# Performance work log

Hardware: AMD Instinct MI355X
Metric: run time of the kernel (lower is better)

The kernel has to match this reference:

```python
import jax, jax.numpy as jnp
import numpy as np

D_MODEL, N_HEADS = 768, 12
D_K = D_MODEL // N_HEADS
NEG = -1e9


def setup_inputs() -> dict:
    key = jax.random.key(0)
    ks = jax.random.split(key, 12)
    B, S, D = 2, 4096, D_MODEL
    s = 1.0 / np.sqrt(D)
    inp = {
        'query': jax.random.normal(ks[0], (B, S, D), jnp.float32),
        'key': jax.random.normal(ks[1], (B, S, D), jnp.float32),
        'value': jax.random.normal(ks[2], (B, S, D), jnp.float32),
        'mask': jnp.ones((B, S), jnp.int32),
        'Wq': jax.random.normal(ks[3], (D, D), jnp.float32) * s,
        'bq': jnp.zeros((D,), jnp.float32),
        'Wk': jax.random.normal(ks[4], (D, D), jnp.float32) * s,
        'bk': jnp.zeros((D,), jnp.float32),
        'Wv': jax.random.normal(ks[5], (D, D), jnp.float32) * s,
        'bv': jnp.zeros((D,), jnp.float32),
        'Wo': jax.random.normal(ks[6], (D, D), jnp.float32) * s,
        'bo': jnp.zeros((D,), jnp.float32),
    }
    return inp


def reference(query, key, value, mask, Wq, bq, Wk, bk, Wv, bv, Wo, bo):
    B, Sq, D = query.shape
    Sk = key.shape[1]
    # torch Linear: x @ W.T + b; weights stored [out, in]
    def proj(x, W, b, S):
        return (x @ W.T + b).reshape(B, S, N_HEADS, D_K).transpose(0, 2, 1, 3)
    Q = proj(query, Wq, bq, Sq)   # [B,H,Sq,Dk]
    K = proj(key, Wk, bk, Sk)
    V = proj(value, Wv, bv, Sk)
    scores = jnp.einsum('bhqd,bhkd->bhqk', Q, K) / jnp.sqrt(jnp.float32(D_K))
    # padding mask on keys: [B,1,1,Sk]
    scores = jnp.where(mask[:, None, None, :] == 0, NEG, scores)
    # causal mask (triu, diagonal=1)
    causal = jnp.triu(jnp.ones((Sq, Sk), bool), k=1)
    scores = jnp.where(causal[None, None], NEG, scores)
    attn = jax.nn.softmax(scores, axis=-1)
    out = jnp.einsum('bhqk,bhkd->bhqd', attn, V)
    out = out.transpose(0, 2, 1, 3).reshape(B, Sq, D)
    return out @ Wo.T + bo
```

## Files before the change

### kernel.cpp

```cpp
#include <hip/hip_runtime.h>
#include <hip/hip_bf16.h>

#define D_MODEL 768
#define N_HEADS 12
#define D_K     64
#define NEG_INF (-1e9f)
#define SCALE_Q 0.1803368801111154f
#define W_ELEMS (D_MODEL * D_MODEL)

typedef __attribute__((ext_vector_type(8))) short          bf16x8;
typedef __attribute__((ext_vector_type(4))) float          floatx4;
typedef __attribute__((ext_vector_type(4))) unsigned short ushortx4;
typedef __attribute__((ext_vector_type(2))) unsigned int   uintx2;
typedef __attribute__((ext_vector_type(4))) unsigned int   uintx4;

static __device__ __forceinline__ unsigned short f2bf(float f) {
    unsigned u = __builtin_bit_cast(unsigned, f);
    u += 0x7FFFu + ((u >> 16) & 1u);
    return (unsigned short)(u >> 16);
}

static __device__ __forceinline__ float exp2_hw(float x) {
#if __has_builtin(__builtin_amdgcn_exp2f)
    return __builtin_amdgcn_exp2f(x);
#else
    return __builtin_exp2f(x);
#endif
}

static __device__ __forceinline__ float rcp_hw(float x) {
#if __has_builtin(__builtin_amdgcn_rcpf)
    return __builtin_amdgcn_rcpf(x);
#else
    return 1.f / x;
#endif
}

static __device__ __forceinline__ void gload_lds16(const void* g, void* l) {
    __builtin_amdgcn_global_load_lds(
        (const __attribute__((address_space(1))) void*)g,
        (__attribute__((address_space(3))) void*)l, 16, 0, 0);
}

__global__ __launch_bounds__(256) void convert_w4(
    const float* __restrict__ W0, const float* __restrict__ W1,
    const float* __restrict__ W2, const float* __restrict__ W3,
    unsigned short* __restrict__ out)
{
    const float* src[4] = {W0, W1, W2, W3};
    const float* W = src[blockIdx.y];
    unsigned short* o = out + (size_t)blockIdx.y * W_ELEMS;
    const int i = (blockIdx.x * 256 + threadIdx.x) * 4;
    float4 v = *(const float4*)(W + i);
    ushortx4 h = { f2bf(v.x), f2bf(v.y), f2bf(v.z), f2bf(v.w) };
    *(ushortx4*)(o + i) = h;
}

__global__ __launch_bounds__(256) void convert_a3(
    const float* __restrict__ A0, const float* __restrict__ A1,
    const float* __restrict__ A2,
    unsigned short* __restrict__ O0, unsigned short* __restrict__ O1,
    unsigned short* __restrict__ O2)
{
    const int z = blockIdx.y;
    const float* A = (z == 0) ? A0 : (z == 1) ? A1 : A2;
    unsigned short* O = (z == 0) ? O0 : (z == 1) ? O1 : O2;
    const int i = (blockIdx.x * 256 + threadIdx.x) * 4;
    float4 v = *(const float4*)(A + i);
    ushortx4 h = { f2bf(v.x), f2bf(v.y), f2bf(v.z), f2bf(v.w) };
    *(ushortx4*)(O + i) = h;
}

__global__ __launch_bounds__(256) void gemm128(
    const unsigned short* __restrict__ A0, const unsigned short* __restrict__ A1,
    const unsigned short* __restrict__ A2,
    const unsigned short* __restrict__ W0, const unsigned short* __restrict__ W1,
    const unsigned short* __restrict__ W2,
    const float* __restrict__ b0, const float* __restrict__ b1,
    const float* __restrict__ b2,
    void* __restrict__ C0, void* __restrict__ C1, void* __restrict__ C2,
    int S)
{
    __shared__ __align__(16) unsigned short As[2][128 * 32];
    __shared__ __align__(16) unsigned short Bs[2][128 * 32];

    const int z = blockIdx.z;
    const unsigned short* A = (z == 0) ? A0 : (z == 1) ? A1 : A2;
    const unsigned short* W = (z == 0) ? W0 : (z == 1) ? W1 : W2;
    const float* bias       = (z == 0) ? b0 : (z == 1) ? b1 : b2;
    void* C                 = (z == 0) ? C0 : (z == 1) ? C1 : C2;
    const float scale = (z == 0) ? SCALE_Q : 1.0f;
    const int mode = (z == 2) ? 3 : 1;

    const int tid  = threadIdx.x;
    const int wave = tid >> 6;
    const int lane = tid & 63;
    const int quad = lane >> 4;
    const int l16  = lane & 15;
    const int m0 = blockIdx.x * 128;
    const int n0 = blockIdx.y * 128;
    const int wm = (wave & 1) * 64;
    const int wn = (wave >> 1) * 64;
    const int sr = lane >> 2;
    const int sc = (lane & 3) << 3;

    const floatx4 zero4 = {0.f, 0.f, 0.f, 0.f};
    floatx4 acc[4][4];
    #pragma unroll
    for (int i = 0; i < 4; ++i)
        #pragma unroll
        for (int j = 0; j < 4; ++j) acc[i][j] = zero4;

    #pragma unroll
    for (int c = 0; c < 2; ++c) {
        const int row = wave * 32 + c * 16;
        gload_lds16(A + (size_t)(m0 + row + sr) * D_MODEL + sc,
                    As[0] + row * 32);
        gload_lds16(W + (size_t)(n0 + row + sr) * D_MODEL + sc,
                    Bs[0] + row * 32);
    }
    __syncthreads();

    const int NI = D_MODEL / 32;
    for (int it = 0; it < NI; ++it) {
        const int cur = it & 1;

        if (it + 1 < NI) {
            const int kn = (it + 1) * 32;
            #pragma unroll
            for (int c = 0; c < 2; ++c) {
                const int row = wave * 32 + c * 16;
                gload_lds16(A + (size_t)(m0 + row + sr) * D_MODEL + kn + sc,
                            As[cur ^ 1] + row * 32);
                gload_lds16(W + (size_t)(n0 + row + sr) * D_MODEL + kn + sc,
                            Bs[cur ^ 1] + row * 32);
            }
        }

        bf16x8 af[4], bfr[4];
        #pragma unroll
        for (int i = 0; i < 4; ++i)
            af[i] = *(const bf16x8*)(As[cur] + (wm + i * 16 + l16) * 32 + quad * 8);
        #pragma unroll
        for (int j = 0; j < 4; ++j)
            bfr[j] = *(const bf16x8*)(Bs[cur] + (wn + j * 16 + l16) * 32 + quad * 8);
        #pragma unroll
        for (int i = 0; i < 4; ++i)
            #pragma unroll
            for (int j = 0; j < 4; ++j)
                acc[i][j] = __builtin_amdgcn_mfma_f32_16x16x32_bf16(
                    bfr[j], af[i], acc[i][j], 0, 0, 0);
        __syncthreads();
    }

    #pragma unroll
    for (int i = 0; i < 4; ++i) {
        const int m = m0 + wm + i * 16 + l16;
        #pragma unroll
        for (int j = 0; j < 4; ++j) {
            const int nb = n0 + wn + j * 16 + quad * 4;
            const float4 bv = *(const float4*)(bias + nb);
            float v0 = (acc[i][j][0] + bv.x) * scale;
            float v1 = (acc[i][j][1] + bv.y) * scale;
            float v2 = (acc[i][j][2] + bv.z) * scale;
            float v3 = (acc[i][j][3] + bv.w) * scale;
            if (mode == 1) {
                ushortx4 o = {f2bf(v0), f2bf(v1), f2bf(v2), f2bf(v3)};
                *(ushortx4*)((unsigned short*)C + (size_t)m * D_MODEL + nb) = o;
            } else {
                const int bb = m / S, s = m - bb * S;
                const int hh = nb >> 6, d = nb & 63;
                unsigned short* base = (unsigned short*)C +
                    ((size_t)(bb * N_HEADS + hh) * D_K + d) * S + s;
                base[0]         = f2bf(v0);
                base[(size_t)S]     = f2bf(v1);
                base[(size_t)S * 2] = f2bf(v2);
                base[(size_t)S * 3] = f2bf(v3);
            }
        }
    }
}

__global__ __launch_bounds__(256) void gemm64o(
    const unsigned short* __restrict__ A,
    const unsigned short* __restrict__ W,
    const float* __restrict__ bias,
    float* __restrict__ C)
{
    __shared__ __align__(16) unsigned short As[2][64 * 32];
    __shared__ __align__(16) unsigned short Bs[2][128 * 32];

    const int tid  = threadIdx.x;
    const int wave = tid >> 6;
    const int lane = tid & 63;
    const int quad = lane >> 4;
    const int l16  = lane & 15;
    const int m0 = blockIdx.x * 64;
    const int n0 = blockIdx.y * 128;
    const int wn = wave * 32;
    const int sr = lane >> 2;
    const int sc = (lane & 3) << 3;

    const floatx4 zero4 = {0.f, 0.f, 0.f, 0.f};
    floatx4 acc[4][2];
    #pragma unroll
    for (int i = 0; i < 4; ++i)
        #pragma unroll
        for (int j = 0; j < 2; ++j) acc[i][j] = zero4;

    {
        if (wave < 2) {
            const int g0 = wave * 32;
            gload_lds16(A + (size_t)(m0 + g0 + sr) * D_MODEL + sc,
                        As[0] + g0 * 32);
            gload_lds16(A + (size_t)(m0 + g0 + 16 + sr) * D_MODEL + sc,
                        As[0] + (g0 + 16) * 32);
            const int bg = 96 + wave * 16;
            gload_lds16(W + (size_t)(n0 + bg + sr) * D_MODEL + sc,
                        Bs[0] + bg * 32);
        } else {
            const int bg = (wave - 2) * 48;
            #pragma unroll
            for (int c = 0; c < 3; ++c)
                gload_lds16(W + (size_t)(n0 + bg + c * 16 + sr) * D_MODEL + sc,
                            Bs[0] + (bg + c * 16) * 32);
        }
    }
    __syncthreads();

    const int NI = D_MODEL / 32;
    for (int it = 0; it < NI; ++it) {
        const int cur = it & 1;

        if (it + 1 < NI) {
            const int kn = (it + 1) * 32;
            if (wave < 2) {
                const int g0 = wave * 32;
                gload_lds16(A + (size_t)(m0 + g0 + sr) * D_MODEL + kn + sc,
                            As[cur ^ 1] + g0 * 32);
                gload_lds16(A + (size_t)(m0 + g0 + 16 + sr) * D_MODEL + kn + sc,
                            As[cur ^ 1] + (g0 + 16) * 32);
                const int bg = 96 + wave * 16;
                gload_lds16(W + (size_t)(n0 + bg + sr) * D_MODEL + kn + sc,
                            Bs[cur ^ 1] + bg * 32);
            } else {
                const int bg = (wave - 2) * 48;
                #pragma unroll
                for (int c = 0; c < 3; ++c)
                    gload_lds16(W + (size_t)(n0 + bg + c * 16 + sr) * D_MODEL + kn + sc,
                                Bs[cur ^ 1] + (bg + c * 16) * 32);
            }
        }

        bf16x8 af[4], bfr[2];
        #pragma unroll
        for (int i = 0; i < 4; ++i)
            af[i] = *(const bf16x8*)(As[cur] + (i * 16 + l16) * 32 + quad * 8);
        #pragma unroll
        for (int j = 0; j < 2; ++j)
            bfr[j] = *(const bf16x8*)(Bs[cur] + (wn + j * 16 + l16) * 32 + quad * 8);
        #pragma unroll
        for (int i = 0; i < 4; ++i)
            #pragma unroll
            for (int j = 0; j < 2; ++j)
                acc[i][j] = __builtin_amdgcn_mfma_f32_16x16x32_bf16(
                    bfr[j], af[i], acc[i][j], 0, 0, 0);
        __syncthreads();
    }

    #pragma unroll
    for (int i = 0; i < 4; ++i) {
        const int m = m0 + i * 16 + l16;
        #pragma unroll
        for (int j = 0; j < 2; ++j) {
            const int nb = n0 + wn + j * 16 + quad * 4;
            const float4 bv = *(const float4*)(bias + nb);
            float4 o = {acc[i][j][0] + bv.x, acc[i][j][1] + bv.y,
                        acc[i][j][2] + bv.z, acc[i][j][3] + bv.w};
            *(float4*)(C + (size_t)m * D_MODEL + nb) = o;
        }
    }
}

__global__ __launch_bounds__(256) void flash_attn(
    const unsigned short* __restrict__ Qp,
    const unsigned short* __restrict__ Kp,
    const unsigned short* __restrict__ VpT,
    const int* __restrict__ mask,
    unsigned short* __restrict__ O,
    int S)
{
    __shared__ __align__(16) unsigned short Ks [2][64 * 64];
    __shared__ __align__(16) unsigned short Vts[2][64 * 64];
    __shared__ __align__(16) float mskf[2][64];

    const int L  = blockIdx.x;
    const int bh = L % 24;
    const int p  = L / 24;
    const int h  = bh % 12;
    const int b  = bh / 12;
    const int nqt = S >> 6;
    const int tid  = threadIdx.x;
    const int wave = tid >> 6;
    const int lane = tid & 63;
    const int quad = lane >> 4;
    const int l16  = lane & 15;
    const int sx   = (l16 & 7) << 3;
    const int qh   = wave & 1;
    const int kh2  = wave >> 1;

    const unsigned short* Kbase = Kp  + (size_t)(b * S) * D_MODEL + h * D_K;
    const unsigned short* Vbase = VpT + (size_t)(b * N_HEADS + h) * D_K * S;
    const int* mbase = mask + b * S;

    const int srow = wave * 8 + (lane >> 3);
    const int sgc  = ((lane & 7) ^ (lane >> 3)) << 3;

    const floatx4 zero4 = {0.f, 0.f, 0.f, 0.f};
    const short one_bf = (short)0x3F80;
    const bf16x8 ones = {one_bf, one_bf, one_bf, one_bf,
                         one_bf, one_bf, one_bf, one_bf};

    #pragma unroll
    for (int sel = 0; sel < 2; ++sel) {
        const int qt = sel ? (nqt - 1 - p) : p;
        const int q0 = qt * 64;

        bf16x8 qf[2][2];
        #pragma unroll
        for (int qg = 0; qg < 2; ++qg) {
            const size_t rowQ =
                (size_t)(b * S + q0 + qh * 32 + qg * 16 + l16) * D_MODEL + h * D_K;
            qf[qg][0] = *(const bf16x8*)(Qp + rowQ + quad * 8);
            qf[qg][1] = *(const bf16x8*)(Qp + rowQ + 32 + quad * 8);
        }

        floatx4 acc2[2][4];
        floatx4 accl[2];
        #pragma unroll
        for (int qg = 0; qg < 2; ++qg) {
            accl[qg] = zero4;
            #pragma unroll
            for (int dt = 0; dt < 4; ++dt) acc2[qg][dt] = zero4;
        }

        const int ni = qt + 1;

        #pragma unroll
        for (int c = 0; c < 2; ++c) {
            gload_lds16(Kbase + (size_t)(c * 32 + srow) * D_MODEL + sgc,
                        (char*)Ks[0] + (c * 4 + wave) * 1024);
            gload_lds16(Vbase + (size_t)(c * 32 + srow) * S + sgc,
                        (char*)Vts[0] + (c * 4 + wave) * 1024);
        }
        if (tid < 64) mskf[0][tid] = (mbase[tid] == 0) ? NEG_INF : 0.f;
        __syncthreads();

        for (int kt = 0; kt < ni; ++kt) {
            const int k0 = kt * 64;
            const int cur = kt & 1;

            if (kt + 1 < ni) {
                const int kn = k0 + 64;
                #pragma unroll
                for (int c = 0; c < 2; ++c) {
                    gload_lds16(
                        Kbase + (size_t)(kn + c * 32 + srow) * D_MODEL + sgc,
                        (char*)Ks[cur ^ 1] + (c * 4 + wave) * 1024);
                    gload_lds16(
                        Vbase + (size_t)(c * 32 + srow) * S + kn + sgc,
                        (char*)Vts[cur ^ 1] + (c * 4 + wave) * 1024);
                }
                if (tid < 64)
                    mskf[cur ^ 1][tid] = (mbase[kn + tid] == 0) ? NEG_INF : 0.f;
            }

            floatx4 s[2][2];
            __builtin_amdgcn_s_setprio(1);
            #pragma unroll
            for (int nt = 0; nt < 2; ++nt) {
                const int krow = kh2 * 32 + nt * 16 + l16;
                const unsigned short* kro = Ks[cur] + krow * 64;
                const bf16x8 kf0 = *(const bf16x8*)(kro + ((quad * 8) ^ sx));
                const bf16x8 kf1 = *(const bf16x8*)(kro + ((32 + quad * 8) ^ sx));
                const floatx4 cm =
                    *(const floatx4*)(&mskf[cur][kh2 * 32 + nt * 16 + quad * 4]);
                #pragma unroll
                for (int qg = 0; qg < 2; ++qg) {
                    floatx4 c = cm;
                    c = __builtin_amdgcn_mfma_f32_16x16x32_bf16(kf0, qf[qg][0], c, 0, 0, 0);
                    c = __builtin_amdgcn_mfma_f32_16x16x32_bf16(kf1, qf[qg][1], c, 0, 0, 0);
                    s[nt][qg] = c;
                }
            }
            __builtin_amdgcn_s_setprio(0);

            if (kt == ni - 1) {
                #pragma unroll
                for (int nt = 0; nt < 2; ++nt) {
                    const int kb = k0 + kh2 * 32 + nt * 16 + quad * 4;
                    #pragma unroll
                    for (int qg = 0; qg < 2; ++qg) {
                        const int qa = q0 + qh * 32 + qg * 16 + l16;
                        #pragma unroll
                        for (int r = 0; r < 4; ++r)
                            if (kb + r > qa) s[nt][qg][r] = NEG_INF;
                    }
                }
            }

            unsigned pk0[2][2], pk1[2][2];
            #pragma unroll
            for (int nt = 0; nt < 2; ++nt)
                #pragma unroll
                for (int qg = 0; qg < 2; ++qg) {
                    const float e0 = exp2_hw(s[nt][qg][0]);
                    const float e1 = exp2_hw(s[nt][qg][1]);
                    const float e2 = exp2_hw(s[nt][qg][2]);
                    const float e3 = exp2_hw(s[nt][qg][3]);
                    pk0[nt][qg] = __builtin_amdgcn_perm(
                        __builtin_bit_cast(unsigned, e1),
                        __builtin_bit_cast(unsigned, e0), 0x07060302u);
                    pk1[nt][qg] = __builtin_amdgcn_perm(
                        __builtin_bit_cast(unsigned, e3),
                        __builtin_bit_cast(unsigned, e2), 0x07060302u);
                }

            bf16x8 pf[2];
            #pragma unroll
            for (int qg = 0; qg < 2; ++qg) {
                uintx2 a32 = __builtin_amdgcn_permlane32_swap(
                    pk0[0][qg], pk0[1][qg], false, false);
                uintx2 b32 = __builtin_amdgcn_permlane32_swap(
                    pk1[0][qg], pk1[1][qg], false, false);
                uintx2 a16 = __builtin_amdgcn_permlane16_swap(
                    a32[0], a32[1], false, false);
                uintx2 b16 = __builtin_amdgcn_permlane16_swap(
                    b32[0], b32[1], false, false);
                const uintx4 pw = {a16[0], b16[0], a16[1], b16[1]};
                pf[qg] = __builtin_bit_cast(bf16x8, pw);
            }
            __builtin_amdgcn_s_setprio(1);
            #pragma unroll
            for (int dt = 0; dt < 4; ++dt) {
                const int vcol = (kh2 * 32 + quad * 8) ^ sx;
                const bf16x8 vf =
                    *(const bf16x8*)(Vts[cur] + (dt * 16 + l16) * 64 + vcol);
                #pragma unroll
                for (int qg = 0; qg < 2; ++qg)
                    acc2[qg][dt] = __builtin_amdgcn_mfma_f32_16x16x32_bf16(
                        pf[qg], vf, acc2[qg][dt], 0, 0, 0);
            }
            #pragma unroll
            for (int qg = 0; qg < 2; ++qg)
                accl[qg] = __builtin_amdgcn_mfma_f32_16x16x32_bf16(
                    pf[qg], ones, accl[qg], 0, 0, 0);
            __builtin_amdgcn_s_setprio(0);

            __syncthreads();
        }

        float* Kf = (float*)Ks;
        float* Vf = (float*)Vts;
        if (kh2 == 1) {
            #pragma unroll
            for (int qg = 0; qg < 2; ++qg) {
                #pragma unroll
                for (int dt = 0; dt < 4; ++dt)
                    *(floatx4*)(Kf + (qh * 8 + qg * 4 + dt) * 256 + lane * 4) =
                        acc2[qg][dt];
                *(floatx4*)(Vf + (qh * 2 + qg) * 256 + lane * 4) = accl[qg];
            }
        }
        __syncthreads();
        if (kh2 == 0) {
            #pragma unroll
            for (int qg = 0; qg < 2; ++qg) {
                accl[qg] += *(const floatx4*)(Vf + (qh * 2 + qg) * 256 + lane * 4);
                #pragma unroll
                for (int dt = 0; dt < 4; ++dt)
                    acc2[qg][dt] +=
                        *(const floatx4*)(Kf + (qh * 8 + qg * 4 + dt) * 256 + lane * 4);
                #pragma unroll
                for (int r = 0; r < 4; ++r) {
                    const float inv = rcp_hw(accl[qg][r]);
                    const int gq = q0 + qh * 32 + qg * 16 + quad * 4 + r;
                    const size_t base = (size_t)(b * S + gq) * D_MODEL + h * D_K;
                    #pragma unroll
                    for (int dt = 0; dt < 4; ++dt)
                        O[base + dt * 16 + l16] = f2bf(acc2[qg][dt][r] * inv);
                }
            }
        }
        __syncthreads();
    }
}

extern "C" void kernel_launch(void* const* d_in, const int* in_sizes, int n_in,
                              void* d_out, int out_size, void* d_ws, size_t ws_size,
                              hipStream_t stream) {
    const float* query = (const float*)d_in[0];
    const float* key   = (const float*)d_in[1];
    const float* value = (const float*)d_in[2];
    const int*   mask  = (const int*)d_in[3];
    const float* Wq = (const float*)d_in[4];
    const float* bq = (const float*)d_in[5];
    const float* Wk = (const float*)d_in[6];
    const float* bk = (const float*)d_in[7];
    const float* Wv = (const float*)d_in[8];
    const float* bv = (const float*)d_in[9];
    const float* Wo = (const float*)d_in[10];
    const float* bo = (const float*)d_in[11];

    const int B  = 2;
    const int BS = in_sizes[3];
    const int S  = BS / B;
    const int M  = BS;

    unsigned short* Qp  = (unsigned short*)d_ws;
    unsigned short* Kp  = Qp  + (size_t)M * D_MODEL;
    unsigned short* VpT = Kp  + (size_t)M * D_MODEL;
    unsigned short* Obf = VpT + (size_t)M * D_MODEL;
    unsigned short* Wbf = Obf + (size_t)M * D_MODEL;
    unsigned short* Wqb = Wbf;
    unsigned short* Wkb = Wbf + (size_t)W_ELEMS;
    unsigned short* Wvb = Wbf + (size_t)W_ELEMS * 2;
    unsigned short* Wob = Wbf + (size_t)W_ELEMS * 3;
    unsigned short* ka = (unsigned short*)d_out;
    unsigned short* va = ka + (size_t)M * D_MODEL;

    dim3 blk(256);
    convert_w4<<<dim3(W_ELEMS / 1024, 4), blk, 0, stream>>>(Wq, Wk, Wv, Wo, Wbf);
    convert_a3<<<dim3((M * D_MODEL) / 1024, 3), blk, 0, stream>>>(
        query, key, value, Obf, ka, va);

    gemm128<<<dim3(M / 128, D_MODEL / 128, 3), blk, 0, stream>>>(
        Obf, ka, va, Wqb, Wkb, Wvb, bq, bk, bv, Qp, Kp, VpT, S);

    flash_attn<<<768, blk, 0, stream>>>(Qp, Kp, VpT, mask, Obf, S);

    gemm64o<<<dim3(M / 64, D_MODEL / 128), blk, 0, stream>>>(
        Obf, Wob, bo, (float*)d_out);
}
```

Baseline: 285.3 us.

## Fuse fp32-to-bf16 activation conversion into the QKV projection GEMM loader

Drops the separate convert_a3 kernel and has the QKV GEMM read fp32 query/key/value straight from global memory. It converts them to bf16 in registers and writes them into the LDS A tile, issuing the loads for the next tile before the MFMAs and the converts after them. This removes one launch plus a full bf16 write and re-read of three activation tensors. In exchange the A tile now moves twice the bytes per tile, goes through registers instead of async global-to-LDS loads, and each tile is converted once per N-block (6 times) rather than once.

```diff
diff --git a/kernel.cpp b/kernel.cpp
--- a/kernel.cpp
+++ b/kernel.cpp
@@ -56,24 +56,9 @@
     *(ushortx4*)(o + i) = h;
 }
 
-__global__ __launch_bounds__(256) void convert_a3(
+__global__ __launch_bounds__(256) void gemm128(
     const float* __restrict__ A0, const float* __restrict__ A1,
     const float* __restrict__ A2,
-    unsigned short* __restrict__ O0, unsigned short* __restrict__ O1,
-    unsigned short* __restrict__ O2)
-{
-    const int z = blockIdx.y;
-    const float* A = (z == 0) ? A0 : (z == 1) ? A1 : A2;
-    unsigned short* O = (z == 0) ? O0 : (z == 1) ? O1 : O2;
-    const int i = (blockIdx.x * 256 + threadIdx.x) * 4;
-    float4 v = *(const float4*)(A + i);
-    ushortx4 h = { f2bf(v.x), f2bf(v.y), f2bf(v.z), f2bf(v.w) };
-    *(ushortx4*)(O + i) = h;
-}
-
-__global__ __launch_bounds__(256) void gemm128(
-    const unsigned short* __restrict__ A0, const unsigned short* __restrict__ A1,
-    const unsigned short* __restrict__ A2,
     const unsigned short* __restrict__ W0, const unsigned short* __restrict__ W1,
     const unsigned short* __restrict__ W2,
     const float* __restrict__ b0, const float* __restrict__ b1,
@@ -85,7 +70,7 @@
     __shared__ __align__(16) unsigned short Bs[2][128 * 32];
 
     const int z = blockIdx.z;
-    const unsigned short* A = (z == 0) ? A0 : (z == 1) ? A1 : A2;
+    const float* A          = (z == 0) ? A0 : (z == 1) ? A1 : A2;
     const unsigned short* W = (z == 0) ? W0 : (z == 1) ? W1 : W2;
     const float* bias       = (z == 0) ? b0 : (z == 1) ? b1 : b2;
     void* C                 = (z == 0) ? C0 : (z == 1) ? C1 : C2;
@@ -114,26 +99,36 @@
     #pragma unroll
     for (int c = 0; c < 2; ++c) {
         const int row = wave * 32 + c * 16;
-        gload_lds16(A + (size_t)(m0 + row + sr) * D_MODEL + sc,
-                    As[0] + row * 32);
         gload_lds16(W + (size_t)(n0 + row + sr) * D_MODEL + sc,
                     Bs[0] + row * 32);
+        const float* srcA = A + (size_t)(m0 + row + sr) * D_MODEL + sc;
+        const float4 v0 = *(const float4*)(srcA);
+        const float4 v1 = *(const float4*)(srcA + 4);
+        ushortx4 h0 = {f2bf(v0.x), f2bf(v0.y), f2bf(v0.z), f2bf(v0.w)};
+        ushortx4 h1 = {f2bf(v1.x), f2bf(v1.y), f2bf(v1.z), f2bf(v1.w)};
+        unsigned short* dst = As[0] + (row + sr) * 32 + sc;
+        *(ushortx4*)(dst)     = h0;
+        *(ushortx4*)(dst + 4) = h1;
     }
     __syncthreads();
 
     const int NI = D_MODEL / 32;
     for (int it = 0; it < NI; ++it) {
         const int cur = it & 1;
-
-        if (it + 1 < NI) {
+        const bool pre = (it + 1 < NI);
+        float4 av[2][2];
+
+        if (pre) {
             const int kn = (it + 1) * 32;
             #pragma unroll
             for (int c = 0; c < 2; ++c) {
                 const int row = wave * 32 + c * 16;
-                gload_lds16(A + (size_t)(m0 + row + sr) * D_MODEL + kn + sc,
-                            As[cur ^ 1] + row * 32);
                 gload_lds16(W + (size_t)(n0 + row + sr) * D_MODEL + kn + sc,
                             Bs[cur ^ 1] + row * 32);
+                const float* srcA =
+                    A + (size_t)(m0 + row + sr) * D_MODEL + kn + sc;
+                av[c][0] = *(const float4*)(srcA);
+                av[c][1] = *(const float4*)(srcA + 4);
             }
         }
 
@@ -150,6 +145,20 @@
             for (int j = 0; j < 4; ++j)
                 acc[i][j] = __builtin_amdgcn_mfma_f32_16x16x32_bf16(
                     bfr[j], af[i], acc[i][j], 0, 0, 0);
+
+        if (pre) {
+            #pragma unroll
+            for (int c = 0; c < 2; ++c) {
+                const int row = wave * 32 + c * 16;
+                ushortx4 h0 = {f2bf(av[c][0].x), f2bf(av[c][0].y),
+                               f2bf(av[c][0].z), f2bf(av[c][0].w)};
+                ushortx4 h1 = {f2bf(av[c][1].x), f2bf(av[c][1].y),
+                               f2bf(av[c][1].z), f2bf(av[c][1].w)};
+                unsigned short* dst = As[cur ^ 1] + (row + sr) * 32 + sc;
+                *(ushortx4*)(dst)     = h0;
+                *(ushortx4*)(dst + 4) = h1;
+            }
+        }
         __syncthreads();
     }
 
@@ -526,16 +535,12 @@
     unsigned short* Wkb = Wbf + (size_t)W_ELEMS;
     unsigned short* Wvb = Wbf + (size_t)W_ELEMS * 2;
     unsigned short* Wob = Wbf + (size_t)W_ELEMS * 3;
-    unsigned short* ka = (unsigned short*)d_out;
-    unsigned short* va = ka + (size_t)M * D_MODEL;
 
     dim3 blk(256);
     convert_w4<<<dim3(W_ELEMS / 1024, 4), blk, 0, stream>>>(Wq, Wk, Wv, Wo, Wbf);
-    convert_a3<<<dim3((M * D_MODEL) / 1024, 3), blk, 0, stream>>>(
-        query, key, value, Obf, ka, va);
 
     gemm128<<<dim3(M / 128, D_MODEL / 128, 3), blk, 0, stream>>>(
-        Obf, ka, va, Wqb, Wkb, Wvb, bq, bk, bv, Qp, Kp, VpT, S);
+        query, key, value, Wqb, Wkb, Wvb, bq, bk, bv, Qp, Kp, VpT, S);
 
     flash_attn<<<768, blk, 0, stream>>>(Qp, Kp, VpT, mask, Obf, S);
 
```

Result: slower. 297.6 us (+4.3%).
